# Kernel tuning notes

Measured on AMD Instinct MI355X. Metric: run time of the kernel, lower is better.

The kernel has to match this reference:

```python
import jax, jax.numpy as jnp
import numpy as np

N = 100000      # nodes
E = 3200000     # edges (avg degree 32)
IN = 256        # in_features
OUT = 128       # out_features


def setup_inputs() -> dict:
    key = jax.random.key(0)
    k_x, k_r, k_c, k_v, k_w, k_b = jax.random.split(key, 6)
    x = jax.random.normal(k_x, (N, IN), dtype=jnp.float32)
    row = jax.random.randint(k_r, (E,), 0, N)          # destination node of each edge
    col = jax.random.randint(k_c, (E,), 0, N)          # source node of each edge
    adj_vals = jax.random.uniform(k_v, (E,), dtype=jnp.float32)  # sparse adj values
    stdv = 1.0 / np.sqrt(OUT)                          # matches reset_parameters
    weight = jax.random.uniform(k_w, (IN, OUT), dtype=jnp.float32, minval=-stdv, maxval=stdv)
    bias = jax.random.uniform(k_b, (OUT,), dtype=jnp.float32, minval=-stdv, maxval=stdv)
    return {"x": x, "adj_vals": adj_vals, "weight": weight, "bias": bias,
            "row": row, "col": col}


def reference(x, adj_vals, weight, bias, row, col):
    # support = input @ W                       [N, OUT]
    support = x @ weight
    # output = spmm(adj, support): for each edge (r, c, v): out[r] += v * support[c]
    gathered = adj_vals[:, None] * support[col]  # [E, OUT] irregular gather
    out = jax.ops.segment_sum(gathered, row, num_segments=N)  # [N, OUT] scatter-add
    return out + bias
```

## Files before the change

### kernel.cpp

```cpp
#include <hip/hip_runtime.h>

#define INF 256
#define OUTF 128
#define NBMAX 1024
#define BUCKET_CAP 4608

typedef _Float16 half2v __attribute__((ext_vector_type(2)));
typedef _Float16 half8 __attribute__((ext_vector_type(8)));
typedef float f32x4 __attribute__((ext_vector_type(4)));

__device__ inline unsigned short f16bits(float v) {
    union { unsigned short u; _Float16 h; } cv;
    cv.h = (_Float16)v;
    return cv.u;
}
__device__ inline float f16val15(unsigned rec) {
    union { unsigned short u; _Float16 h; } cv;
    cv.u = (unsigned short)(rec << 1);
    return (float)cv.h;
}

__global__ __launch_bounds__(256) void k_prepack(const float* __restrict__ w,
                                                 _Float16* __restrict__ wpack,
                                                 int* __restrict__ bcursor,
                                                 int NB) {
    int t = blockIdx.x * 256 + threadIdx.x;
    int k = t >> 7, n = t & 127;
    int ks = k >> 5, quad = (k >> 3) & 3, j = k & 7;
    int ct = n >> 4, nn = n & 15;
    wpack[(((ks * 8 + ct) * 4 + quad) * 16 + nn) * 8 + j] = (_Float16)w[k * OUTF + n];
    if (t < NB) bcursor[t] = t * BUCKET_CAP;
}

__global__ __launch_bounds__(256) void gcn_gemm_mfma(const float* __restrict__ x,
                                                     const _Float16* __restrict__ wpack,
                                                     _Float16* __restrict__ support,
                                                     int N) {
    const int tid = threadIdx.x;
    const int wv = tid >> 6;
    const int lane = tid & 63;
    const int m16 = lane & 15;
    const int quad = lane >> 4;
    const int rowbase = blockIdx.x * 128 + wv * 32;

    f32x4 acc[2][8];
#pragma unroll
    for (int rt = 0; rt < 2; ++rt)
#pragma unroll
        for (int ct = 0; ct < 8; ++ct)
            acc[rt][ct] = (f32x4){0.f, 0.f, 0.f, 0.f};

    int r0 = rowbase + m16;
    int r1 = rowbase + 16 + m16;
    int r0c = (r0 < N) ? r0 : N - 1;
    int r1c = (r1 < N) ? r1 : N - 1;
    const float* xr0 = x + (long)r0c * INF + quad * 8;
    const float* xr1 = x + (long)r1c * INF + quad * 8;

    for (int ks = 0; ks < 8; ++ks) {
        float4 u0 = *(const float4*)(xr0 + ks * 32);
        float4 v0 = *(const float4*)(xr0 + ks * 32 + 4);
        float4 u1 = *(const float4*)(xr1 + ks * 32);
        float4 v1 = *(const float4*)(xr1 + ks * 32 + 4);
        half8 a0 = {(_Float16)u0.x, (_Float16)u0.y, (_Float16)u0.z, (_Float16)u0.w,
                    (_Float16)v0.x, (_Float16)v0.y, (_Float16)v0.z, (_Float16)v0.w};
        half8 a1 = {(_Float16)u1.x, (_Float16)u1.y, (_Float16)u1.z, (_Float16)u1.w,
                    (_Float16)v1.x, (_Float16)v1.y, (_Float16)v1.z, (_Float16)v1.w};

        half8 b[8];
#pragma unroll
        for (int ct = 0; ct < 8; ++ct)
            b[ct] = *(const half8*)(wpack + (size_t)(((ks * 8 + ct) * 4 + quad) * 16 + m16) * 8);

#pragma unroll
        for (int ct = 0; ct < 8; ++ct) {
            acc[0][ct] = __builtin_amdgcn_mfma_f32_16x16x32_f16(a0, b[ct], acc[0][ct], 0, 0, 0);
            acc[1][ct] = __builtin_amdgcn_mfma_f32_16x16x32_f16(a1, b[ct], acc[1][ct], 0, 0, 0);
        }
    }

#pragma unroll
    for (int rt = 0; rt < 2; ++rt) {
        int rb = rowbase + rt * 16 + quad * 4;
#pragma unroll
        for (int reg = 0; reg < 4; ++reg) {
            int r = rb + reg;
            if (r < N) {
#pragma unroll
                for (int ct = 0; ct < 8; ++ct)
                    support[(long)r * OUTF + ct * 16 + m16] = (_Float16)acc[rt][ct][reg];
            }
        }
    }
}

__global__ __launch_bounds__(256) void k_coarse_scatter(const int* __restrict__ row,
                                                        const int* __restrict__ col,
                                                        const float* __restrict__ vals,
                                                        int* __restrict__ bcursor,
                                                        uint2* __restrict__ tmp,
                                                        int NB, int E) {
    __shared__ int cnt[NBMAX];
    __shared__ int sbase[NBMAX];
    const int tid = threadIdx.x;
    for (int i = tid; i < NB; i += 256) cnt[i] = 0;
    __syncthreads();

    int b[16], rk[16];
    uint2 rec[16];
    int base = blockIdx.x * 4096;
#pragma unroll
    for (int j = 0; j < 16; ++j) {
        int e = base + j * 256 + tid;
        if (e < E) {
            int r = row[e];
            int c = col[e];
            float v = vals[e];
            rec[j].x = ((unsigned)r << 15) | ((unsigned)f16bits(v) >> 1);
            rec[j].y = (unsigned)c;
            b[j] = r >> 7;
            rk[j] = atomicAdd(&cnt[b[j]], 1);
        } else {
            b[j] = -1;
        }
    }
    __syncthreads();
    for (int i = tid; i < NB; i += 256) {
        int c = cnt[i];
        if (c) sbase[i] = atomicAdd(&bcursor[i], c);
    }
    __syncthreads();
#pragma unroll
    for (int j = 0; j < 16; ++j) {
        if (b[j] >= 0) tmp[sbase[b[j]] + rk[j]] = rec[j];
    }
}

__global__ __launch_bounds__(256) void k_bucket_sort(const uint2* __restrict__ tmp,
                                                     const int* __restrict__ bcursor,
                                                     unsigned* __restrict__ frecs,
                                                     int* __restrict__ rs,
                                                     int* __restrict__ re,
                                                     int N) {
    __shared__ uint2 recs[BUCKET_CAP];
    __shared__ int cnt[128];
    __shared__ int offs[128];

    const int tid = threadIdx.x;
    const int b = blockIdx.x;
    const int start = b * BUCKET_CAP;
    int n = bcursor[b] - start;
    if (n > BUCKET_CAP) n = BUCKET_CAP;
    const int row0 = b << 7;

    if (tid < 128) cnt[tid] = 0;
    __syncthreads();

    for (int i = tid; i < n; i += 256) {
        uint2 r = tmp[start + i];
        recs[i] = r;
        atomicAdd(&cnt[(r.x >> 15) & 127], 1);
    }
    __syncthreads();

    if (tid < 128) offs[tid] = cnt[tid];
    __syncthreads();
    for (int d = 1; d < 128; d <<= 1) {
        int add = 0;
        if (tid < 128 && tid >= d) add = offs[tid - d];
        __syncthreads();
        if (tid < 128) offs[tid] += add;
        __syncthreads();
    }
    if (tid < 128) {
        int excl = offs[tid] - cnt[tid];
        offs[tid] = excl;
        int r = row0 + tid;
        if (r < N) {
            rs[r] = start + excl;
            re[r] = start + excl + cnt[tid];
        }
    }
    __syncthreads();

    for (int i = tid; i < n; i += 256) {
        uint2 r = recs[i];
        int lr = (r.x >> 15) & 127;
        int pos = atomicAdd(&offs[lr], 1);
        frecs[start + pos] = (r.y << 15) | (r.x & 0x7FFF);
    }
}

__global__ __launch_bounds__(256) void k_gather(const half2v* __restrict__ sup,
                                                const unsigned* __restrict__ frecs,
                                                const int* __restrict__ rs,
                                                const int* __restrict__ re,
                                                const float* __restrict__ bias,
                                                float* __restrict__ out,
                                                int N) {
    int wid = (blockIdx.x * 256 + threadIdx.x) >> 6;
    int lane = threadIdx.x & 63;
    if (wid >= N) return;

    int start = rs[wid];
    int end = re[wid];

    float ax = 0.f, ay = 0.f;
    int i = start;
    for (; i + 4 <= end; i += 4) {
        unsigned r0 = frecs[i + 0], r1 = frecs[i + 1];
        unsigned r2 = frecs[i + 2], r3 = frecs[i + 3];
        float v0 = f16val15(r0), v1 = f16val15(r1);
        float v2 = f16val15(r2), v3 = f16val15(r3);
        half2v h0 = sup[(long)(r0 >> 15) * 64 + lane];
        half2v h1 = sup[(long)(r1 >> 15) * 64 + lane];
        half2v h2 = sup[(long)(r2 >> 15) * 64 + lane];
        half2v h3 = sup[(long)(r3 >> 15) * 64 + lane];
        ax += v0 * (float)h0.x + v1 * (float)h1.x + v2 * (float)h2.x + v3 * (float)h3.x;
        ay += v0 * (float)h0.y + v1 * (float)h1.y + v2 * (float)h2.y + v3 * (float)h3.y;
    }
    for (; i < end; ++i) {
        unsigned r = frecs[i];
        float v = f16val15(r);
        half2v h = sup[(long)(r >> 15) * 64 + lane];
        ax += v * (float)h.x;
        ay += v * (float)h.y;
    }

    float2 bb = ((const float2*)bias)[lane];
    float2 o;
    o.x = ax + bb.x;
    o.y = ay + bb.y;
    ((float2*)out)[(long)wid * 64 + lane] = o;
}

extern "C" void kernel_launch(void* const* d_in, const int* in_sizes, int n_in,
                              void* d_out, int out_size, void* d_ws, size_t ws_size,
                              hipStream_t stream) {
    const float* x    = (const float*)d_in[0];
    const float* vals = (const float*)d_in[1];
    const float* w    = (const float*)d_in[2];
    const float* bias = (const float*)d_in[3];
    const int*   row  = (const int*)d_in[4];
    const int*   col  = (const int*)d_in[5];

    const int N = in_sizes[0] / INF;
    const int E = in_sizes[1];
    const int NB = (N + 127) / 128;

    char* p = (char*)d_ws;
    _Float16* support = (_Float16*)p;  p += (size_t)N * OUTF * sizeof(_Float16);
    unsigned* frecs   = (unsigned*)p;  p += (size_t)NB * BUCKET_CAP * sizeof(unsigned);
    _Float16* wpack   = (_Float16*)p;  p += (size_t)INF * OUTF * sizeof(_Float16);
    int* rs           = (int*)p;       p += (size_t)N * sizeof(int);
    int* re           = (int*)p;       p += (size_t)N * sizeof(int);
    int* bcursor      = (int*)p;       p += (size_t)NBMAX * sizeof(int);

    uint2* tmp = (uint2*)d_out;

    const int eb4096 = (E + 4095) / 4096;

    k_prepack<<<(INF * OUTF) / 256, 256, 0, stream>>>(w, wpack, bcursor, NB);

    gcn_gemm_mfma<<<(N + 127) / 128, 256, 0, stream>>>(x, wpack, support, N);

    k_coarse_scatter<<<eb4096, 256, 0, stream>>>(row, col, vals, bcursor, tmp, NB, E);

    k_bucket_sort<<<NB, 256, 0, stream>>>(tmp, bcursor, frecs, rs, re, N);

    {
        int blocks = (N * 64 + 255) / 256;
        k_gather<<<blocks, 256, 0, stream>>>((const half2v*)support, frecs,
                                             rs, re, bias, (float*)d_out, N);
    }
}
```

Baseline: 411.6 us.

## Store support in feature slabs and gather per slab; split scatter temp records

The GEMM now writes support as eight column slabs of 16 features each. Gather blocks are assigned to one slab for a 128-row bucket, so each slab (about 3.2MB in fp16) can stay in L2/LLC while it is reused. Within a wave, eight edge slots each read a 32-byte chunk, and partial sums are reduced with shuffles. Temporary scatter records shrink from 8 bytes to a 4-byte col/value word plus a 1-byte local row, which cuts sort traffic. In exchange, each destination row's edge list is read eight times, there are more small uncoalesced 32B reads, and the shuffle reductions add overhead.

Measured after the change: 634.0 us. 1.54x slower.

```diff
diff --git a/kernel.cpp b/kernel.cpp
--- a/kernel.cpp
+++ b/kernel.cpp
@@ -88,7 +88,7 @@
             if (r < N) {
 #pragma unroll
                 for (int ct = 0; ct < 8; ++ct)
-                    support[(long)r * OUTF + ct * 16 + m16] = (_Float16)acc[rt][ct][reg];
+                    support[((size_t)ct * N + r) * 16 + m16] = (_Float16)acc[rt][ct][reg];
             }
         }
     }
@@ -98,7 +98,8 @@
                                                         const int* __restrict__ col,
                                                         const float* __restrict__ vals,
                                                         int* __restrict__ bcursor,
-                                                        uint2* __restrict__ tmp,
+                                                        unsigned* __restrict__ cv_tmp,
+                                                        unsigned char* __restrict__ lr_tmp,
                                                         int NB, int E) {
     __shared__ int cnt[NBMAX];
     __shared__ int sbase[NBMAX];
@@ -106,22 +107,19 @@
     for (int i = tid; i < NB; i += 256) cnt[i] = 0;
     __syncthreads();
 
-    int b[16], rk[16];
-    uint2 rec[16];
+    int rr[16], rk[16];
+    unsigned rec[16];
     int base = blockIdx.x * 4096;
 #pragma unroll
     for (int j = 0; j < 16; ++j) {
         int e = base + j * 256 + tid;
         if (e < E) {
             int r = row[e];
-            int c = col[e];
-            float v = vals[e];
-            rec[j].x = ((unsigned)r << 15) | ((unsigned)f16bits(v) >> 1);
-            rec[j].y = (unsigned)c;
-            b[j] = r >> 7;
-            rk[j] = atomicAdd(&cnt[b[j]], 1);
+            rec[j] = ((unsigned)col[e] << 15) | ((unsigned)f16bits(vals[e]) >> 1);
+            rr[j] = r;
+            rk[j] = atomicAdd(&cnt[r >> 7], 1);
         } else {
-            b[j] = -1;
+            rr[j] = -1;
         }
     }
     __syncthreads();
@@ -132,17 +130,23 @@
     __syncthreads();
 #pragma unroll
     for (int j = 0; j < 16; ++j) {
-        if (b[j] >= 0) tmp[sbase[b[j]] + rk[j]] = rec[j];
-    }
-}
-
-__global__ __launch_bounds__(256) void k_bucket_sort(const uint2* __restrict__ tmp,
+        if (rr[j] >= 0) {
+            int pos = sbase[rr[j] >> 7] + rk[j];
+            cv_tmp[pos] = rec[j];
+            lr_tmp[pos] = (unsigned char)(rr[j] & 127);
+        }
+    }
+}
+
+__global__ __launch_bounds__(256) void k_bucket_sort(const unsigned* __restrict__ cv_tmp,
+                                                     const unsigned char* __restrict__ lr_tmp,
                                                      const int* __restrict__ bcursor,
                                                      unsigned* __restrict__ frecs,
                                                      int* __restrict__ rs,
                                                      int* __restrict__ re,
                                                      int N) {
-    __shared__ uint2 recs[BUCKET_CAP];
+    __shared__ unsigned recs[BUCKET_CAP];
+    __shared__ unsigned char lrows[BUCKET_CAP];
     __shared__ int cnt[128];
     __shared__ int offs[128];
 
@@ -157,9 +161,11 @@
     __syncthreads();
 
     for (int i = tid; i < n; i += 256) {
-        uint2 r = tmp[start + i];
-        recs[i] = r;
-        atomicAdd(&cnt[(r.x >> 15) & 127], 1);
+        unsigned c = cv_tmp[start + i];
+        unsigned char l = lr_tmp[start + i];
+        recs[i] = c;
+        lrows[i] = l;
+        atomicAdd(&cnt[l], 1);
     }
     __syncthreads();
 
@@ -184,54 +190,55 @@
     __syncthreads();
 
     for (int i = tid; i < n; i += 256) {
-        uint2 r = recs[i];
-        int lr = (r.x >> 15) & 127;
-        int pos = atomicAdd(&offs[lr], 1);
-        frecs[start + pos] = (r.y << 15) | (r.x & 0x7FFF);
-    }
-}
-
-__global__ __launch_bounds__(256) void k_gather(const half2v* __restrict__ sup,
-                                                const unsigned* __restrict__ frecs,
-                                                const int* __restrict__ rs,
-                                                const int* __restrict__ re,
-                                                const float* __restrict__ bias,
-                                                float* __restrict__ out,
-                                                int N) {
-    int wid = (blockIdx.x * 256 + threadIdx.x) >> 6;
-    int lane = threadIdx.x & 63;
-    if (wid >= N) return;
-
-    int start = rs[wid];
-    int end = re[wid];
-
-    float ax = 0.f, ay = 0.f;
-    int i = start;
-    for (; i + 4 <= end; i += 4) {
-        unsigned r0 = frecs[i + 0], r1 = frecs[i + 1];
-        unsigned r2 = frecs[i + 2], r3 = frecs[i + 3];
-        float v0 = f16val15(r0), v1 = f16val15(r1);
-        float v2 = f16val15(r2), v3 = f16val15(r3);
-        half2v h0 = sup[(long)(r0 >> 15) * 64 + lane];
-        half2v h1 = sup[(long)(r1 >> 15) * 64 + lane];
-        half2v h2 = sup[(long)(r2 >> 15) * 64 + lane];
-        half2v h3 = sup[(long)(r3 >> 15) * 64 + lane];
-        ax += v0 * (float)h0.x + v1 * (float)h1.x + v2 * (float)h2.x + v3 * (float)h3.x;
-        ay += v0 * (float)h0.y + v1 * (float)h1.y + v2 * (float)h2.y + v3 * (float)h3.y;
-    }
-    for (; i < end; ++i) {
-        unsigned r = frecs[i];
-        float v = f16val15(r);
-        half2v h = sup[(long)(r >> 15) * 64 + lane];
-        ax += v * (float)h.x;
-        ay += v * (float)h.y;
-    }
-
-    float2 bb = ((const float2*)bias)[lane];
-    float2 o;
-    o.x = ax + bb.x;
-    o.y = ay + bb.y;
-    ((float2*)out)[(long)wid * 64 + lane] = o;
+        int l = lrows[i];
+        int pos = atomicAdd(&offs[l], 1);
+        frecs[start + pos] = recs[i];
+    }
+}
+
+__global__ __launch_bounds__(256) void k_gather_slab(const _Float16* __restrict__ slabs,
+                                                     const unsigned* __restrict__ frecs,
+                                                     const int* __restrict__ rs,
+                                                     const int* __restrict__ re,
+                                                     const float* __restrict__ bias,
+                                                     float* __restrict__ out,
+                                                     int N) {
+    const int tid = threadIdx.x;
+    const int b = blockIdx.x >> 3;
+    const int g = blockIdx.x & 7;
+    const int wv = tid >> 6;
+    const int lane = tid & 63;
+    const int eslot = lane >> 3;
+    const int fpair = lane & 7;
+    const _Float16* slab = slabs + (size_t)g * N * 16;
+    const int row0 = (b << 7) + wv * 32;
+
+    float2 bb = *(const float2*)(bias + g * 16 + fpair * 2);
+
+    for (int rrow = 0; rrow < 32; ++rrow) {
+        int r = row0 + rrow;
+        if (r >= N) break;
+        int s = rs[r], e = re[r];
+
+        float ax = 0.f, ay = 0.f;
+        for (int i = s + eslot; i < e; i += 8) {
+            unsigned rec = frecs[i];
+            float v = f16val15(rec);
+            unsigned c = rec >> 15;
+            half2v h = *(const half2v*)(slab + (size_t)c * 16 + fpair * 2);
+            ax += v * (float)h.x;
+            ay += v * (float)h.y;
+        }
+        ax += __shfl_down(ax, 32); ay += __shfl_down(ay, 32);
+        ax += __shfl_down(ax, 16); ay += __shfl_down(ay, 16);
+        ax += __shfl_down(ax, 8);  ay += __shfl_down(ay, 8);
+        if (eslot == 0) {
+            float2 o;
+            o.x = ax + bb.x;
+            o.y = ay + bb.y;
+            *(float2*)(out + (size_t)r * OUTF + g * 16 + fpair * 2) = o;
+        }
+    }
 }
 
 extern "C" void kernel_launch(void* const* d_in, const int* in_sizes, int n_in,
@@ -256,7 +263,8 @@
     int* re           = (int*)p;       p += (size_t)N * sizeof(int);
     int* bcursor      = (int*)p;       p += (size_t)NBMAX * sizeof(int);
 
-    uint2* tmp = (uint2*)d_out;
+    unsigned* cv_tmp      = (unsigned*)d_out;
+    unsigned char* lr_tmp = (unsigned char*)d_out + (size_t)NB * BUCKET_CAP * sizeof(unsigned);
 
     const int eb4096 = (E + 4095) / 4096;
 
@@ -264,13 +272,11 @@
 
     gcn_gemm_mfma<<<(N + 127) / 128, 256, 0, stream>>>(x, wpack, support, N);
 
-    k_coarse_scatter<<<eb4096, 256, 0, stream>>>(row, col, vals, bcursor, tmp, NB, E);
-
-    k_bucket_sort<<<NB, 256, 0, stream>>>(tmp, bcursor, frecs, rs, re, N);
-
-    {
-        int blocks = (N * 64 + 255) / 256;
-        k_gather<<<blocks, 256, 0, stream>>>((const half2v*)support, frecs,
-                                             rs, re, bias, (float*)d_out, N);
-    }
-}
+    k_coarse_scatter<<<eb4096, 256, 0, stream>>>(row, col, vals, bcursor,
+                                                 cv_tmp, lr_tmp, NB, E);
+
+    k_bucket_sort<<<NB, 256, 0, stream>>>(cv_tmp, lr_tmp, bcursor, frecs, rs, re, N);
+
+    k_gather_slab<<<NB * 8, 256, 0, stream>>>(support, frecs, rs, re, bias,
+                                              (float*)d_out, N);
+}
```
